# Kernel tuning notes

Measured on AMD Instinct MI355X. Metric: run time of the kernel, lower is better.

Reference implementation:

```python
import jax, jax.numpy as jnp
import numpy as np

DIM = 256
HEADS = 8
DIM_HEAD = 32
HIDDEN = HEADS * DIM_HEAD  # 256
SCALE = DIM_HEAD ** -0.5


def setup_inputs() -> dict:
    key = jax.random.key(0)
    k1, k2, k3, k4 = jax.random.split(key, 4)
    x = jax.random.normal(k1, (1, DIM, 16, 16, 16), dtype=jnp.float32)
    # 1x1x1 Conv3d weights are plain channel-mixing matrices
    w_qkv = jax.random.normal(k2, (3 * HIDDEN, DIM), dtype=jnp.float32) * (DIM ** -0.5)
    w_out = jax.random.normal(k3, (DIM, HIDDEN), dtype=jnp.float32) * (HIDDEN ** -0.5)
    b_out = jax.random.normal(k4, (DIM,), dtype=jnp.float32) * 0.01
    return {"x": x, "w_qkv": w_qkv, "w_out": w_out, "b_out": b_out}


def reference(x, w_qkv, w_out, b_out):
    b, c, X, Y, Z = x.shape
    n = X * Y * Z
    xf = x.reshape(b, c, n)                                   # b c n
    qkv = jnp.einsum('oc,bcn->bon', w_qkv, xf)                # b 3H n
    q, k, v = jnp.split(qkv, 3, axis=1)                       # each b (h c) n
    def heads(t):
        return t.reshape(b, HEADS, DIM_HEAD, n)               # b h c n
    q, k, v = heads(q) * SCALE, heads(k), heads(v)
    sim = jnp.einsum('bhci,bhcj->bhij', q, k)                 # b h n n
    attn = jax.nn.softmax(sim, axis=-1)
    out = jnp.einsum('bhij,bhcj->bhci', attn, v)              # b h c n
    out = out.reshape(b, HIDDEN, n)                           # b (h c) n
    out = jnp.einsum('oc,bcn->bon', w_out, out) + b_out[None, :, None]
    return out.reshape(b, DIM, X, Y, Z)
```

## Files before the change

kernel.cpp:

```cpp
#include <hip/hip_runtime.h>
#include <hip/hip_bf16.h>
#include <cstdint>


typedef __bf16 bf16x8 __attribute__((ext_vector_type(8)));
typedef float f32x4 __attribute__((ext_vector_type(4)));
typedef float f32x16 __attribute__((ext_vector_type(16)));
typedef unsigned int u32;
typedef unsigned short u16;
typedef u32 u32x4v __attribute__((ext_vector_type(4)));
typedef u32 u32x2v __attribute__((ext_vector_type(2)));

#define MFMA16(a, b, c) __builtin_amdgcn_mfma_f32_16x16x32_bf16(a, b, c, 0, 0, 0)
#define MFMA32(a, b, c) __builtin_amdgcn_mfma_f32_32x32x16_bf16(a, b, c, 0, 0, 0)

#if __has_builtin(__builtin_amdgcn_exp2f)
#define EXP2(x) __builtin_amdgcn_exp2f(x)
#else
#define EXP2(x) exp2f(x)
#endif

__device__ __forceinline__ u16 f2bf(float f) {
  __bf16 b = (__bf16)f;
  return __builtin_bit_cast(u16, b);
}
__device__ __forceinline__ u32 pk2(float a, float b) {
  return (u32)f2bf(a) | ((u32)f2bf(b) << 16);
}
__device__ __forceinline__ bf16x8 ldfrag(const u16* p) {
  return __builtin_bit_cast(bf16x8, *(const u32x4v*)p);
}
__device__ __forceinline__ void gload_lds16(const void* g, void* l) {
  __builtin_amdgcn_global_load_lds((const __attribute__((address_space(1))) u32*)g,
                                   (__attribute__((address_space(3))) u32*)l, 16, 0, 0);
}
__device__ __forceinline__ void plswap(u32& a, u32& b) {
  asm("v_permlane32_swap_b32 %0, %1" : "+v"(a), "+v"(b));
}
__device__ __forceinline__ f32x16 zero16() {
  f32x16 z;
#pragma unroll
  for (int i = 0; i < 16; ++i) z[i] = 0.0f;
  return z;
}

#if __has_builtin(__builtin_amdgcn_fdot2_f32_bf16)
typedef __bf16 bf16x2 __attribute__((ext_vector_type(2)));
__device__ __forceinline__ float dot2one(u32 pk, float acc) {
  const u32 one2 = 0x3F803F80u;
  return __builtin_amdgcn_fdot2_f32_bf16(__builtin_bit_cast(bf16x2, pk),
                                         __builtin_bit_cast(bf16x2, one2), acc, false);
}
#define LSUM_STEP(LSUM, P, PK)                               \
  {                                                          \
    _Pragma("unroll") for (int m_ = 0; m_ < 8; ++m_) LSUM =  \
        dot2one(PK[m_], LSUM);                               \
  }
#else
#define LSUM_STEP(LSUM, P, PK)                               \
  {                                                          \
    float t0_ = (P[0] + P[1]) + (P[2] + P[3]);               \
    float t1_ = (P[4] + P[5]) + (P[6] + P[7]);               \
    float t2_ = (P[8] + P[9]) + (P[10] + P[11]);             \
    float t3_ = (P[12] + P[13]) + (P[14] + P[15]);           \
    LSUM += (t0_ + t1_) + (t2_ + t3_);                       \
  }
#endif

__global__ __launch_bounds__(256) void prep(const float* __restrict__ x,
                                            const float* __restrict__ wq,
                                            const float* __restrict__ wo,
                                            u16* __restrict__ xT, u16* __restrict__ wqb,
                                            u16* __restrict__ wob) {
  const int b = blockIdx.x;
  const int t = threadIdx.x;
  if (b < 256) {
    __shared__ u16 tile[64][72];
    const int n0 = (b & 63) * 64, c0 = (b >> 6) * 64;
#pragma unroll
    for (int r = 0; r < 4; ++r) {
      int c = r * 16 + (t >> 4);
      int n4 = (t & 15) << 2;
      float4 v = *(const float4*)(x + (size_t)(c0 + c) * 4096 + n0 + n4);
      tile[n4 + 0][c] = f2bf(v.x);
      tile[n4 + 1][c] = f2bf(v.y);
      tile[n4 + 2][c] = f2bf(v.z);
      tile[n4 + 3][c] = f2bf(v.w);
    }
    __syncthreads();
#pragma unroll
    for (int r2 = 0; r2 < 2; ++r2) {
      int n = r2 * 32 + (t >> 3);
      int c8 = (t & 7) << 3;
      u32x4v o;
#pragma unroll
      for (int j = 0; j < 4; ++j)
        o[j] = (u32)tile[n][c8 + 2 * j] | ((u32)tile[n][c8 + 2 * j + 1] << 16);
      *(u32x4v*)(xT + (size_t)(n0 + n) * 256 + c0 + c8) = o;
    }
  } else if (b < 304) {
    int base = (b - 256) * 4096;
#pragma unroll
    for (int r = 0; r < 4; ++r) {
      int i = base + r * 1024 + t * 4;
      float4 v = *(const float4*)(wq + i);
      float sc = (i < 65536) ? 0.2550349f : 1.0f;
      u32x2v pkd;
      pkd.x = pk2(v.x * sc, v.y * sc);
      pkd.y = pk2(v.z * sc, v.w * sc);
      *(u32x2v*)(wqb + i) = pkd;
    }
  } else {
    int base = (b - 304) * 4096;
#pragma unroll
    for (int r = 0; r < 4; ++r) {
      int i = base + r * 1024 + t * 4;
      float4 v = *(const float4*)(wo + i);
      u32x2v pkd;
      pkd.x = pk2(v.x, v.y);
      pkd.y = pk2(v.z, v.w);
      *(u32x2v*)(wob + i) = pkd;
    }
  }
}

__global__ __launch_bounds__(256) void qkv_gemm(const u16* __restrict__ xT,
                                                const u16* __restrict__ wqb,
                                                u16* __restrict__ qT, u16* __restrict__ kT,
                                                u16* __restrict__ vv) {
  __shared__ __align__(16) u16 Al[64 * 64];
  __shared__ __align__(16) u16 Bl[64 * 64];
  const int t = threadIdx.x;
  const int lane = t & 63, w = t >> 6;
  const int wm = w & 1, wn = w >> 1;
  const int o0 = blockIdx.y * 64, n0 = blockIdx.x * 64;
  const int lr = lane & 15, lg = lane >> 4;
  const int srow = lane >> 3, sslot = lane & 7;
  f32x4 acc[2][2];
#pragma unroll
  for (int i = 0; i < 2; ++i)
#pragma unroll
    for (int j = 0; j < 2; ++j)
#pragma unroll
      for (int r = 0; r < 4; ++r) acc[i][j][r] = 0.0f;

  for (int kc = 0; kc < 256; kc += 64) {
#pragma unroll
    for (int rnd = 0; rnd < 2; ++rnd) {
      int row = rnd * 32 + w * 8 + srow;
      gload_lds16(wqb + (size_t)(o0 + row) * 256 + kc + ((sslot ^ (row & 7)) << 3),
                  (void*)(Al + rnd * 2048 + w * 512));
      gload_lds16(xT + (size_t)(n0 + row) * 256 + kc + ((sslot ^ (row & 7)) << 3),
                  (void*)(Bl + rnd * 2048 + w * 512));
    }
    __syncthreads();
#pragma unroll
    for (int kk = 0; kk < 2; ++kk) {
      bf16x8 af[2], bf_[2];
#pragma unroll
      for (int mi = 0; mi < 2; ++mi) {
        int row = wm * 32 + mi * 16 + lr;
        af[mi] = ldfrag(&Al[row * 64 + ((kk * 32 + lg * 8) ^ ((row & 7) << 3))]);
      }
#pragma unroll
      for (int ni = 0; ni < 2; ++ni) {
        int row = wn * 32 + ni * 16 + lr;
        bf_[ni] = ldfrag(&Bl[row * 64 + ((kk * 32 + lg * 8) ^ ((row & 7) << 3))]);
      }
#pragma unroll
      for (int mi = 0; mi < 2; ++mi)
#pragma unroll
        for (int ni = 0; ni < 2; ++ni) acc[mi][ni] = MFMA16(af[mi], bf_[ni], acc[mi][ni]);
    }
    __syncthreads();
  }
#pragma unroll
  for (int mi = 0; mi < 2; ++mi) {
#pragma unroll
    for (int ni = 0; ni < 2; ++ni) {
      int obase = o0 + wm * 32 + mi * 16 + lg * 4;
      int n = n0 + wn * 32 + ni * 16 + lr;
      int part = obase >> 8;
      int oin = obase & 255;
      int h = oin >> 5, c0 = oin & 31;
      if (part == 0) {
        u32x2v pv;
        pv.x = pk2(acc[mi][ni][0], acc[mi][ni][1]);
        pv.y = pk2(acc[mi][ni][2], acc[mi][ni][3]);
        *(u32x2v*)(qT + ((size_t)h * 4096 + n) * 32 + c0) = pv;
      } else if (part == 1) {
        u32x2v pv;
        pv.x = pk2(acc[mi][ni][0], acc[mi][ni][1]);
        pv.y = pk2(acc[mi][ni][2], acc[mi][ni][3]);
        *(u32x2v*)(kT + ((size_t)h * 4096 + n) * 32 + c0) = pv;
      } else {
#pragma unroll
        for (int r = 0; r < 4; ++r)
          vv[((size_t)h * 32 + c0 + r) * 4096 + n] = f2bf(acc[mi][ni][r]);
      }
    }
  }
}


#define LOAD_TILE(KV0, K0, K1, V0, V1)                            \
  do {                                                            \
    const u16* kp_ = kTh + (size_t)((KV0) + l31) * 32 + lh * 8;   \
    K0 = ldfrag(kp_);                                             \
    K1 = ldfrag(kp_ + 16);                                        \
    const u16* vp_ = vh + (size_t)l31 * 4096 + (KV0) + lh * 8;    \
    V0 = ldfrag(vp_);                                             \
    V1 = ldfrag(vp_ + 16);                                        \
  } while (0)

#define COMPUTE_IT(QF0, QF1, OACC, LSUM, K0, K1, V0, V1)                      \
  do {                                                                        \
    f32x16 sT_ = zero16();                                                    \
    __builtin_amdgcn_s_setprio(1);                                            \
    sT_ = MFMA32(K0, QF0, sT_);                  \
    sT_ = MFMA32(K1, QF1, sT_);                                               \
    __builtin_amdgcn_s_setprio(0);                                            \
    float p_[16];                                                             \
    _Pragma("unroll") for (int r_ = 0; r_ < 16; ++r_) p_[r_] = EXP2(sT_[r_]); \
    u32 pkv_[8];                                                              \
    _Pragma("unroll") for (int m_ = 0; m_ < 8; ++m_) pkv_[m_] =               \
        pk2(p_[2 * m_], p_[2 * m_ + 1]);                                      \
    LSUM_STEP(LSUM, p_, pkv_)                                                 \
    u32 ax_ = pkv_[0], bx_ = pkv_[2];                                         \
    plswap(ax_, bx_);                                                         \
    u32 ay_ = pkv_[1], by_ = pkv_[3];                                         \
    plswap(ay_, by_);                                                         \
    u32 cx_ = pkv_[4], dx_ = pkv_[6];                                         \
    plswap(cx_, dx_);                                                         \
    u32 cy_ = pkv_[5], dy_ = pkv_[7];                                         \
    plswap(cy_, dy_);                                                         \
    u32x4v f1_, f2_;                                                          \
    f1_.x = ax_; f1_.y = ay_; f1_.z = bx_; f1_.w = by_;                       \
    f2_.x = cx_; f2_.y = cy_; f2_.z = dx_; f2_.w = dy_;                       \
    __builtin_amdgcn_s_setprio(1);                                            \
    OACC = MFMA32(V0, __builtin_bit_cast(bf16x8, f1_), OACC);                 \
    OACC = MFMA32(V1, __builtin_bit_cast(bf16x8, f2_), OACC);                 \
    __builtin_amdgcn_s_setprio(0);                                            \
  } while (0)

__global__ __launch_bounds__(512, 4) void attn_fused(const u16* __restrict__ qT,
                                                     const u16* __restrict__ kT,
                                                     const u16* __restrict__ vv,
                                                     u16* __restrict__ aout) {
  __shared__ float pbuf[8 * 32 * 66];
  __shared__ float lbuf[8 * 64];
  const int tid = threadIdx.x;
  const int lane = tid & 63, s = tid >> 6;
  const int qb = blockIdx.x, h = blockIdx.y;
  const int l31 = lane & 31, lh = lane >> 5;
  const u16* qTh = qT + (size_t)h * (4096 * 32);
  const u16* kTh = kT + (size_t)h * (4096 * 32);
  const u16* vh = vv + (size_t)h * (32 * 4096);

  const int i0 = qb * 64 + l31;
  bf16x8 qf00 = ldfrag(qTh + (size_t)i0 * 32 + lh * 8);
  bf16x8 qf01 = ldfrag(qTh + (size_t)i0 * 32 + 16 + lh * 8);
  bf16x8 qf10 = ldfrag(qTh + (size_t)(i0 + 32) * 32 + lh * 8);
  bf16x8 qf11 = ldfrag(qTh + (size_t)(i0 + 32) * 32 + 16 + lh * 8);

  f32x16 oacc0 = zero16(), oacc1 = zero16();
  float lsum0 = 0.0f, lsum1 = 0.0f;
  const int kvbase = s * 512;

  bf16x8 ka0, ka1, va0, va1, kb0, kb1, vb0, vb1;
  LOAD_TILE(kvbase, ka0, ka1, va0, va1);
  for (int tt = 0; tt < 16; tt += 2) {
    LOAD_TILE(kvbase + (tt + 1) * 32, kb0, kb1, vb0, vb1);
    COMPUTE_IT(qf00, qf01, oacc0, lsum0, ka0, ka1, va0, va1);
    COMPUTE_IT(qf10, qf11, oacc1, lsum1, ka0, ka1, va0, va1);
    if (tt + 2 < 16) LOAD_TILE(kvbase + (tt + 2) * 32, ka0, ka1, va0, va1);
    COMPUTE_IT(qf00, qf01, oacc0, lsum0, kb0, kb1, vb0, vb1);
    COMPUTE_IT(qf10, qf11, oacc1, lsum1, kb0, kb1, vb0, vb1);
  }

  float ls0 = lsum0 + __shfl_xor(lsum0, 32, 64);
  float ls1 = lsum1 + __shfl_xor(lsum1, 32, 64);
#pragma unroll
  for (int r = 0; r < 16; ++r) {
    int c = (r & 3) + 8 * (r >> 2) + 4 * lh;
    pbuf[(s * 32 + c) * 66 + l31] = oacc0[r];
    pbuf[(s * 32 + c) * 66 + 32 + l31] = oacc1[r];
  }
  lbuf[s * 64 + l31] = ls0;
  lbuf[s * 64 + 32 + l31] = ls1;
  __syncthreads();

  {
    int i = tid >> 3, c0 = (tid & 7) << 2;
    float lt = 0.0f;
#pragma unroll
    for (int ss = 0; ss < 8; ++ss) lt += lbuf[ss * 64 + i];
    float inv = 1.0f / lt;
    float a[4];
#pragma unroll
    for (int cc = 0; cc < 4; ++cc) a[cc] = 0.0f;
#pragma unroll
    for (int ss = 0; ss < 8; ++ss)
#pragma unroll
      for (int cc = 0; cc < 4; ++cc) a[cc] += pbuf[(ss * 32 + c0 + cc) * 66 + i];
    u32x2v ov;
    ov.x = pk2(a[0] * inv, a[1] * inv);
    ov.y = pk2(a[2] * inv, a[3] * inv);
    *(u32x2v*)(aout + (size_t)(qb * 64 + i) * 256 + h * 32 + c0) = ov;
  }
}

__global__ __launch_bounds__(256) void out_proj(const u16* __restrict__ wob,
                                                const float* __restrict__ bo,
                                                const u16* __restrict__ aout,
                                                float* __restrict__ out) {
  __shared__ __align__(16) u16 Al[64 * 64];
  __shared__ __align__(16) u16 Bl[64 * 64];
  const int t = threadIdx.x;
  const int lane = t & 63, w = t >> 6;
  const int n0 = blockIdx.x * 64, d0 = blockIdx.y * 64;
  const int lr = lane & 15, lg = lane >> 4;
  const int srow = lane >> 3, sslot = lane & 7;
  f32x4 acc[4];
#pragma unroll
  for (int ni = 0; ni < 4; ++ni)
#pragma unroll
    for (int r = 0; r < 4; ++r) acc[ni][r] = 0.0f;

  for (int kc = 0; kc < 256; kc += 64) {
#pragma unroll
    for (int rnd = 0; rnd < 2; ++rnd) {
      int row = rnd * 32 + w * 8 + srow;
      gload_lds16(wob + (size_t)(d0 + row) * 256 + kc + ((sslot ^ (row & 7)) << 3),
                  (void*)(Al + rnd * 2048 + w * 512));
      gload_lds16(aout + (size_t)(n0 + row) * 256 + kc + ((sslot ^ (row & 7)) << 3),
                  (void*)(Bl + rnd * 2048 + w * 512));
    }
    __syncthreads();
#pragma unroll
    for (int kk = 0; kk < 2; ++kk) {
      int arow = w * 16 + lr;
      bf16x8 af = ldfrag(&Al[arow * 64 + ((kk * 32 + lg * 8) ^ ((arow & 7) << 3))]);
#pragma unroll
      for (int ni = 0; ni < 4; ++ni) {
        int brow = ni * 16 + lr;
        bf16x8 bfr = ldfrag(&Bl[brow * 64 + ((kk * 32 + lg * 8) ^ ((brow & 7) << 3))]);
        acc[ni] = MFMA16(af, bfr, acc[ni]);
      }
    }
    __syncthreads();
  }
#pragma unroll
  for (int ni = 0; ni < 4; ++ni) {
    int n = n0 + ni * 16 + lr;
#pragma unroll
    for (int r = 0; r < 4; ++r) {
      int d = d0 + w * 16 + lg * 4 + r;
      out[(size_t)d * 4096 + n] = acc[ni][r] + bo[d];
    }
  }
}

extern "C" void kernel_launch(void* const* d_in, const int* in_sizes, int n_in,
                              void* d_out, int out_size, void* d_ws, size_t ws_size,
                              hipStream_t stream) {
  (void)in_sizes; (void)n_in; (void)out_size; (void)ws_size;
  const float* x = (const float*)d_in[0];
  const float* wqkv = (const float*)d_in[1];
  const float* wout = (const float*)d_in[2];
  const float* bout = (const float*)d_in[3];
  float* out = (float*)d_out;
  u16* qT = (u16*)d_ws;
  u16* kT = qT + 8 * 4096 * 32;
  u16* vv = kT + 8 * 4096 * 32;
  u16* aout = vv + 8 * 32 * 4096;
  u16* xT = aout + 4096 * 256;
  u16* wqb = xT + 4096 * 256;
  u16* wob = wqb + 768 * 256;

  prep<<<320, 256, 0, stream>>>(x, wqkv, wout, xT, wqb, wob);
  qkv_gemm<<<dim3(64, 12), 256, 0, stream>>>(xT, wqb, qT, kT, vv);
  attn_fused<<<dim3(64, 8), 512, 0, stream>>>(qT, kT, vv, aout);
  out_proj<<<dim3(64, 4), 256, 0, stream>>>(wob, bout, aout, out);
}
```

Measured before the change: 52.68 us.

## Halve query rows per attention block, doubling grid and raising occupancy

Each attention block now handles 32 query rows instead of 64, so the grid doubles from 64x8 to 128x8 and launch bounds ask for 8 blocks per CU instead of 4. The inner loop is rewritten to process a single query tile, with the next K/V fragments loaded right after their use, and exp/pack is split into two halves to cut live registers. The aim is more waves in flight on 256 CUs and better latency hiding. The cost is that each K/V fragment is reused by one query tile instead of two, which doubles K/V traffic per unit of work, and the block-level reduction runs twice as often.

```diff
diff --git a/kernel.cpp b/kernel.cpp
--- a/kernel.cpp
+++ b/kernel.cpp
@@ -51,20 +51,13 @@
   return __builtin_amdgcn_fdot2_f32_bf16(__builtin_bit_cast(bf16x2, pk),
                                          __builtin_bit_cast(bf16x2, one2), acc, false);
 }
-#define LSUM_STEP(LSUM, P, PK)                               \
-  {                                                          \
-    _Pragma("unroll") for (int m_ = 0; m_ < 8; ++m_) LSUM =  \
-        dot2one(PK[m_], LSUM);                               \
-  }
+#define LSUM4(LSUM, PK0, PK1, PK2, PK3) \
+  LSUM = dot2one(PK0, LSUM);            \
+  LSUM = dot2one(PK1, LSUM);            \
+  LSUM = dot2one(PK2, LSUM);            \
+  LSUM = dot2one(PK3, LSUM);
 #else
-#define LSUM_STEP(LSUM, P, PK)                               \
-  {                                                          \
-    float t0_ = (P[0] + P[1]) + (P[2] + P[3]);               \
-    float t1_ = (P[4] + P[5]) + (P[6] + P[7]);               \
-    float t2_ = (P[8] + P[9]) + (P[10] + P[11]);             \
-    float t3_ = (P[12] + P[13]) + (P[14] + P[15]);           \
-    LSUM += (t0_ + t1_) + (t2_ + t3_);                       \
-  }
+#define LSUM4(LSUM, PK0, PK1, PK2, PK3)
 #endif
 
 __global__ __launch_bounds__(256) void prep(const float* __restrict__ x,
@@ -202,53 +195,12 @@
   }
 }
 
-
-#define LOAD_TILE(KV0, K0, K1, V0, V1)                            \
-  do {                                                            \
-    const u16* kp_ = kTh + (size_t)((KV0) + l31) * 32 + lh * 8;   \
-    K0 = ldfrag(kp_);                                             \
-    K1 = ldfrag(kp_ + 16);                                        \
-    const u16* vp_ = vh + (size_t)l31 * 4096 + (KV0) + lh * 8;    \
-    V0 = ldfrag(vp_);                                             \
-    V1 = ldfrag(vp_ + 16);                                        \
-  } while (0)
-
-#define COMPUTE_IT(QF0, QF1, OACC, LSUM, K0, K1, V0, V1)                      \
-  do {                                                                        \
-    f32x16 sT_ = zero16();                                                    \
-    __builtin_amdgcn_s_setprio(1);                                            \
-    sT_ = MFMA32(K0, QF0, sT_);                  \
-    sT_ = MFMA32(K1, QF1, sT_);                                               \
-    __builtin_amdgcn_s_setprio(0);                                            \
-    float p_[16];                                                             \
-    _Pragma("unroll") for (int r_ = 0; r_ < 16; ++r_) p_[r_] = EXP2(sT_[r_]); \
-    u32 pkv_[8];                                                              \
-    _Pragma("unroll") for (int m_ = 0; m_ < 8; ++m_) pkv_[m_] =               \
-        pk2(p_[2 * m_], p_[2 * m_ + 1]);                                      \
-    LSUM_STEP(LSUM, p_, pkv_)                                                 \
-    u32 ax_ = pkv_[0], bx_ = pkv_[2];                                         \
-    plswap(ax_, bx_);                                                         \
-    u32 ay_ = pkv_[1], by_ = pkv_[3];                                         \
-    plswap(ay_, by_);                                                         \
-    u32 cx_ = pkv_[4], dx_ = pkv_[6];                                         \
-    plswap(cx_, dx_);                                                         \
-    u32 cy_ = pkv_[5], dy_ = pkv_[7];                                         \
-    plswap(cy_, dy_);                                                         \
-    u32x4v f1_, f2_;                                                          \
-    f1_.x = ax_; f1_.y = ay_; f1_.z = bx_; f1_.w = by_;                       \
-    f2_.x = cx_; f2_.y = cy_; f2_.z = dx_; f2_.w = dy_;                       \
-    __builtin_amdgcn_s_setprio(1);                                            \
-    OACC = MFMA32(V0, __builtin_bit_cast(bf16x8, f1_), OACC);                 \
-    OACC = MFMA32(V1, __builtin_bit_cast(bf16x8, f2_), OACC);                 \
-    __builtin_amdgcn_s_setprio(0);                                            \
-  } while (0)
-
-__global__ __launch_bounds__(512, 4) void attn_fused(const u16* __restrict__ qT,
+__global__ __launch_bounds__(512, 8) void attn_fused(const u16* __restrict__ qT,
                                                      const u16* __restrict__ kT,
                                                      const u16* __restrict__ vv,
                                                      u16* __restrict__ aout) {
-  __shared__ float pbuf[8 * 32 * 66];
-  __shared__ float lbuf[8 * 64];
+  __shared__ float pbuf[8 * 32 * 33];
+  __shared__ float lbuf[8 * 32];
   const int tid = threadIdx.x;
   const int lane = tid & 63, s = tid >> 6;
   const int qb = blockIdx.x, h = blockIdx.y;
@@ -257,56 +209,93 @@
   const u16* kTh = kT + (size_t)h * (4096 * 32);
   const u16* vh = vv + (size_t)h * (32 * 4096);
 
-  const int i0 = qb * 64 + l31;
-  bf16x8 qf00 = ldfrag(qTh + (size_t)i0 * 32 + lh * 8);
-  bf16x8 qf01 = ldfrag(qTh + (size_t)i0 * 32 + 16 + lh * 8);
-  bf16x8 qf10 = ldfrag(qTh + (size_t)(i0 + 32) * 32 + lh * 8);
-  bf16x8 qf11 = ldfrag(qTh + (size_t)(i0 + 32) * 32 + 16 + lh * 8);
-
-  f32x16 oacc0 = zero16(), oacc1 = zero16();
-  float lsum0 = 0.0f, lsum1 = 0.0f;
+  const int i0 = qb * 32 + l31;
+  bf16x8 qf0 = ldfrag(qTh + (size_t)i0 * 32 + lh * 8);
+  bf16x8 qf1 = ldfrag(qTh + (size_t)i0 * 32 + 16 + lh * 8);
+
+  f32x16 oacc = zero16();
+  float lsum = 0.0f;
   const int kvbase = s * 512;
 
-  bf16x8 ka0, ka1, va0, va1, kb0, kb1, vb0, vb1;
-  LOAD_TILE(kvbase, ka0, ka1, va0, va1);
-  for (int tt = 0; tt < 16; tt += 2) {
-    LOAD_TILE(kvbase + (tt + 1) * 32, kb0, kb1, vb0, vb1);
-    COMPUTE_IT(qf00, qf01, oacc0, lsum0, ka0, ka1, va0, va1);
-    COMPUTE_IT(qf10, qf11, oacc1, lsum1, ka0, ka1, va0, va1);
-    if (tt + 2 < 16) LOAD_TILE(kvbase + (tt + 2) * 32, ka0, ka1, va0, va1);
-    COMPUTE_IT(qf00, qf01, oacc0, lsum0, kb0, kb1, vb0, vb1);
-    COMPUTE_IT(qf10, qf11, oacc1, lsum1, kb0, kb1, vb0, vb1);
-  }
-
-  float ls0 = lsum0 + __shfl_xor(lsum0, 32, 64);
-  float ls1 = lsum1 + __shfl_xor(lsum1, 32, 64);
+  const u16* kp = kTh + (size_t)(kvbase + l31) * 32 + lh * 8;
+  const u16* vp = vh + (size_t)l31 * 4096 + kvbase + lh * 8;
+  bf16x8 kf0 = ldfrag(kp), kf1 = ldfrag(kp + 16);
+  bf16x8 vf0 = ldfrag(vp), vf1 = ldfrag(vp + 16);
+
+  for (int tt = 0; tt < 16; ++tt) {
+    kp += 1024;
+    vp += 32;
+    f32x16 sT = zero16();
+    __builtin_amdgcn_s_setprio(1);
+    sT = MFMA32(kf0, qf0, sT);
+    sT = MFMA32(kf1, qf1, sT);
+    __builtin_amdgcn_s_setprio(0);
+    kf0 = ldfrag(kp);
+    kf1 = ldfrag(kp + 16);
+    {
+      float p0 = EXP2(sT[0]), p1 = EXP2(sT[1]), p2 = EXP2(sT[2]), p3 = EXP2(sT[3]);
+      float p4 = EXP2(sT[4]), p5 = EXP2(sT[5]), p6 = EXP2(sT[6]), p7 = EXP2(sT[7]);
+      u32 k0 = pk2(p0, p1), k1 = pk2(p2, p3), k2 = pk2(p4, p5), k3 = pk2(p6, p7);
+#if __has_builtin(__builtin_amdgcn_fdot2_f32_bf16)
+      LSUM4(lsum, k0, k1, k2, k3)
+#else
+      lsum += ((p0 + p1) + (p2 + p3)) + ((p4 + p5) + (p6 + p7));
+#endif
+      u32 ax = k0, bx = k2;
+      plswap(ax, bx);
+      u32 ay = k1, by = k3;
+      plswap(ay, by);
+      u32x4v f1;
+      f1.x = ax; f1.y = ay; f1.z = bx; f1.w = by;
+      __builtin_amdgcn_s_setprio(1);
+      oacc = MFMA32(vf0, __builtin_bit_cast(bf16x8, f1), oacc);
+      __builtin_amdgcn_s_setprio(0);
+    }
+    {
+      float p0 = EXP2(sT[8]), p1 = EXP2(sT[9]), p2 = EXP2(sT[10]), p3 = EXP2(sT[11]);
+      float p4 = EXP2(sT[12]), p5 = EXP2(sT[13]), p6 = EXP2(sT[14]), p7 = EXP2(sT[15]);
+      u32 k0 = pk2(p0, p1), k1 = pk2(p2, p3), k2 = pk2(p4, p5), k3 = pk2(p6, p7);
+#if __has_builtin(__builtin_amdgcn_fdot2_f32_bf16)
+      LSUM4(lsum, k0, k1, k2, k3)
+#else
+      lsum += ((p0 + p1) + (p2 + p3)) + ((p4 + p5) + (p6 + p7));
+#endif
+      u32 cx = k0, dx = k2;
+      plswap(cx, dx);
+      u32 cy = k1, dy = k3;
+      plswap(cy, dy);
+      u32x4v f2;
+      f2.x = cx; f2.y = cy; f2.z = dx; f2.w = dy;
+      __builtin_amdgcn_s_setprio(1);
+      oacc = MFMA32(vf1, __builtin_bit_cast(bf16x8, f2), oacc);
+      __builtin_amdgcn_s_setprio(0);
+    }
+    vf0 = ldfrag(vp);
+    vf1 = ldfrag(vp + 16);
+  }
+
+  float ls = lsum + __shfl_xor(lsum, 32, 64);
 #pragma unroll
   for (int r = 0; r < 16; ++r) {
     int c = (r & 3) + 8 * (r >> 2) + 4 * lh;
-    pbuf[(s * 32 + c) * 66 + l31] = oacc0[r];
-    pbuf[(s * 32 + c) * 66 + 32 + l31] = oacc1[r];
-  }
-  lbuf[s * 64 + l31] = ls0;
-  lbuf[s * 64 + 32 + l31] = ls1;
+    pbuf[(s * 32 + c) * 33 + l31] = oacc[r];
+  }
+  lbuf[s * 32 + l31] = ls;
   __syncthreads();
 
   {
-    int i = tid >> 3, c0 = (tid & 7) << 2;
+    int i = tid >> 4, c0 = (tid & 15) << 1;
     float lt = 0.0f;
 #pragma unroll
-    for (int ss = 0; ss < 8; ++ss) lt += lbuf[ss * 64 + i];
+    for (int ss = 0; ss < 8; ++ss) lt += lbuf[ss * 32 + i];
     float inv = 1.0f / lt;
-    float a[4];
-#pragma unroll
-    for (int cc = 0; cc < 4; ++cc) a[cc] = 0.0f;
-#pragma unroll
-    for (int ss = 0; ss < 8; ++ss)
-#pragma unroll
-      for (int cc = 0; cc < 4; ++cc) a[cc] += pbuf[(ss * 32 + c0 + cc) * 66 + i];
-    u32x2v ov;
-    ov.x = pk2(a[0] * inv, a[1] * inv);
-    ov.y = pk2(a[2] * inv, a[3] * inv);
-    *(u32x2v*)(aout + (size_t)(qb * 64 + i) * 256 + h * 32 + c0) = ov;
+    float a0 = 0.0f, a1 = 0.0f;
+#pragma unroll
+    for (int ss = 0; ss < 8; ++ss) {
+      a0 += pbuf[(ss * 32 + c0) * 33 + i];
+      a1 += pbuf[(ss * 32 + c0 + 1) * 33 + i];
+    }
+    *(u32*)(aout + (size_t)(qb * 32 + i) * 256 + h * 32 + c0) = pk2(a0 * inv, a1 * inv);
   }
 }
 
@@ -380,6 +369,6 @@
 
   prep<<<320, 256, 0, stream>>>(x, wqkv, wout, xT, wqb, wob);
   qkv_gemm<<<dim3(64, 12), 256, 0, stream>>>(xT, wqb, qT, kT, vv);
-  attn_fused<<<dim3(64, 8), 512, 0, stream>>>(qT, kT, vv, aout);
+  attn_fused<<<dim3(128, 8), 512, 0, stream>>>(qT, kT, vv, aout);
   out_proj<<<dim3(64, 4), 256, 0, stream>>>(wob, bout, aout, out);
 }
```

Measured after the change: 68.82 us. 1.31x slower.
